# Kernel tuning notes

Hardware: AMD Instinct MI355X
Metric: run time of the kernel (lower is better)

## Reference

```python
import jax, jax.numpy as jnp
import numpy as np

N, D, E, EDGE_DIM = 8192, 64, 262144, 4


def setup_inputs() -> dict:
    key = jax.random.key(0)
    k1, k2, k3, k4, k5, k6 = jax.random.split(key, 6)
    mag = jax.random.uniform(k1, (N, D), dtype=jnp.float32)
    phase = jax.random.normal(k2, (N, D), dtype=jnp.float32)
    edge_index = jax.random.randint(k3, (2, E), 0, N, dtype=jnp.int64)
    edge_attr = jax.random.normal(k4, (E, EDGE_DIM), dtype=jnp.float32)
    # nn.Linear(edge_dim, hidden_dim): weight [hidden_dim, edge_dim], bias [hidden_dim]
    bound = 1.0 / np.sqrt(EDGE_DIM)
    W = jax.random.uniform(k5, (D, EDGE_DIM), minval=-bound, maxval=bound, dtype=jnp.float32)
    b = jax.random.uniform(k6, (D,), minval=-bound, maxval=bound, dtype=jnp.float32)
    return {"mag": mag, "phase": phase, "edge_index": edge_index,
            "edge_attr": edge_attr, "W": W, "b": b}


def reference(mag, phase, edge_index, edge_attr, W, b):
    # score_ij = sum_d mag_i[d]*mag_j[d]*cos(phase_i[d]-phase_j[d])
    # Via cos(a-b) = cos a cos b + sin a sin b -> two [N,D]@[D,N] matmuls,
    # avoiding the O(N^2 D) intermediate while computing identical math.
    c = mag * jnp.cos(phase)  # [N, D]
    s = mag * jnp.sin(phase)  # [N, D]
    scores = c @ c.T + s @ s.T  # [N, N]
    # edge bias: edge_bias[src, dst] = sum_h Linear(edge_attr)[e, h]
    edge_scores = (edge_attr @ W.T + b).sum(axis=-1)  # [E]
    bias = jnp.zeros((mag.shape[0], mag.shape[0]), dtype=scores.dtype)
    bias = bias.at[edge_index[0], edge_index[1]].set(edge_scores)
    scores = scores + bias
    attn = jax.nn.softmax(scores, axis=1)  # [N, N]
    new_mag = attn @ mag  # [N, D]
    new_phase = attn @ phase  # [N, D]
    return new_mag, new_phase
```

## Files before the change

kernel.cpp:

```cpp
#include <hip/hip_runtime.h>
#include <hip/hip_bf16.h>
#include <cstdint>

#define N_NODES 8192
#define DDIM    64
#define DX      128
#define NEDGE   262144
#define BR      128
#define BC      64
#define SPLITS  8
#define TILES   (N_NODES / BC / SPLITS)
#define RCAP    64
#define MSHIFT  66.0f
#define PSTR    76

typedef float f32x4 __attribute__((ext_vector_type(4)));
typedef short short8 __attribute__((ext_vector_type(8)));

__device__ __forceinline__ short f2bf(float f) {
    union { float f; uint32_t u; } v; v.f = f;
    uint32_t u = v.u;
    uint32_t r = (u + 0x7FFFu + ((u >> 16) & 1u)) >> 16;
    return (short)r;
}
__device__ __forceinline__ float bf2f(short s) {
    union { uint32_t u; float f; } v;
    v.u = ((uint32_t)(uint16_t)s) << 16;
    return v.f;
}

__global__ void cpa_prep_all(const float* __restrict__ mag, const float* __restrict__ phase,
                             const int* __restrict__ ei, const float* __restrict__ ea,
                             const float* __restrict__ W, const float* __restrict__ b,
                             short* __restrict__ Xbf, short* __restrict__ Ybt,
                             float* __restrict__ es, int* __restrict__ cnt,
                             int* __restrict__ keys) {
    __shared__ short tile[64][65];
    __shared__ float wsb[5];
    const int blk = blockIdx.x;
    const int tid = threadIdx.x;
    if (blk < 2048) {
        int idx = blk * 256 + tid;
        int i = idx >> 6, d = idx & 63;
        float m = mag[idx], p = phase[idx];
        Xbf[i * DX + d]      = f2bf(m * __cosf(p));
        Xbf[i * DX + 64 + d] = f2bf(m * __sinf(p));
    } else if (blk < 2304) {
        int bb = blk - 2048;
        int bi = bb >> 1;
        int bc = bb & 1;
        int i0 = bi * 64;
        const float* src = bc ? phase : mag;
        for (int itr = 0; itr < 16; ++itr) {
            int idx = tid + itr * 256;
            int ii = idx >> 6, cc = idx & 63;
            tile[ii][cc] = f2bf(src[(size_t)(i0 + ii) * 64 + cc]);
        }
        __syncthreads();
        for (int itr = 0; itr < 16; ++itr) {
            int idx = tid + itr * 256;
            int cc = idx >> 6, ii = idx & 63;
            Ybt[(size_t)(bc * 64 + cc) * N_NODES + i0 + ii] = tile[ii][cc];
        }
    } else {
        if (tid < 64) {
            float w0 = W[tid * 4 + 0], w1 = W[tid * 4 + 1];
            float w2 = W[tid * 4 + 2], w3 = W[tid * 4 + 3];
            float bb = b[tid];
            #pragma unroll
            for (int o = 32; o > 0; o >>= 1) {
                w0 += __shfl_down(w0, o);
                w1 += __shfl_down(w1, o);
                w2 += __shfl_down(w2, o);
                w3 += __shfl_down(w3, o);
                bb += __shfl_down(bb, o);
            }
            if (tid == 0) { wsb[0] = w0; wsb[1] = w1; wsb[2] = w2; wsb[3] = w3; wsb[4] = bb; }
        }
        __syncthreads();
        int e = (blk - 2304) * 256 + tid;
        float4 a = *(const float4*)(ea + (size_t)e * 4);
        es[e] = a.x * wsb[0] + a.y * wsb[1] + a.z * wsb[2] + a.w * wsb[3] + wsb[4];
        int src = ei[e];
        int dst = ei[NEDGE + e];
        int pos = atomicAdd(&cnt[src], 1);
        if (pos < RCAP) keys[src * RCAP + pos] = (dst << 18) | e;
    }
}

__global__ __launch_bounds__(256) void cpa_sortrows(const int* __restrict__ cnt,
                                                    int* __restrict__ keys) {
    int row  = blockIdx.x * 4 + (threadIdx.x >> 6);
    int lane = threadIdx.x & 63;
    int len  = min(cnt[row], RCAP);
    int base = row * RCAP;
    int v = (lane < len) ? keys[base + lane] : 0x7FFFFFFF;

    #pragma unroll
    for (int k = 2; k <= 64; k <<= 1) {
        #pragma unroll
        for (int j = k >> 1; j >= 1; j >>= 1) {
            int p = __shfl_xor(v, j);
            bool asc = (lane & k) == 0;
            bool low = (lane & j) == 0;
            v = (low == asc) ? min(v, p) : max(v, p);
        }
    }
    int nxt = __shfl_down(v, 1);
    bool dead = (lane + 1 < len) && ((v >> 18) == (nxt >> 18));
    if (lane < len) keys[base + lane] = v | (dead ? 0x80000000 : 0);
}

__global__ __launch_bounds__(512) void cpa_flash(
    const short* __restrict__ Xbf, const short* __restrict__ Ybt,
    const float* __restrict__ es, const int* __restrict__ keys,
    const int* __restrict__ cnt,
    float* __restrict__ lsplit, short* __restrict__ Opart)
{
    __shared__ short Xj[BC][136];
    __shared__ short Yt[DX][72];
    __shared__ short Pl[BR][PSTR];

    const int tid   = threadIdx.x;
    const int lane  = tid & 63;
    const int w     = tid >> 6;
    const int q     = lane >> 4;
    const int colid = lane & 15;

    const int ib = blockIdx.x;
    const int split = blockIdx.y;
    const int i0 = ib * BR;
    const int jstart = split * (N_NODES / SPLITS);

    short8 afrag[4];
    #pragma unroll
    for (int kf = 0; kf < 4; ++kf)
        afrag[kf] = *(const short8*)(Xbf + (size_t)(i0 + w * 16 + colid) * DX + kf * 32 + q * 8);

    int cur = 0, rend = 0;
    if (lane < 16) {
        int i = i0 + w * 16 + lane;
        cur = i * RCAP;
        rend = cur + min(cnt[i], RCAP);
        while (cur < rend) {
            int k = keys[cur];
            int dst = (k >> 18) & 0x1FFF;
            if (dst >= jstart) break;
            ++cur;
        }
    }

    float l_r[4] = {0.f, 0.f, 0.f, 0.f};
    f32x4 O[8];
    #pragma unroll
    for (int t = 0; t < 8; ++t) O[t] = (f32x4){0.f, 0.f, 0.f, 0.f};

    for (int tt = 0; tt < TILES; ++tt) {
        const int j0 = jstart + tt * BC;
        for (int itr = 0; itr < 2; ++itr) {
            int idx = tid + itr * 512;
            int r = idx >> 4;
            int c8 = (idx & 15) << 3;
            *(int4*)(&Xj[r][c8]) = *(const int4*)(Xbf + (size_t)(j0 + r) * DX + c8);
        }
        for (int itr = 0; itr < 2; ++itr) {
            int idx = tid + itr * 512;
            int n = idx >> 3;
            int k8 = (idx & 7) << 3;
            *(int4*)(&Yt[n][k8]) = *(const int4*)(Ybt + (size_t)n * N_NODES + j0 + k8);
        }
        __syncthreads();

        f32x4 S[4];
        #pragma unroll
        for (int st = 0; st < 4; ++st) {
            f32x4 acc = (f32x4){0.f, 0.f, 0.f, 0.f};
            #pragma unroll
            for (int kf = 0; kf < 4; ++kf) {
                short8 bfrag = *(const short8*)&Xj[st * 16 + colid][kf * 32 + q * 8];
                acc = __builtin_amdgcn_mfma_f32_16x16x32_bf16(afrag[kf], bfrag, acc, 0, 0, 0);
            }
            S[st] = acc;
        }
        float rsum[4] = {0.f, 0.f, 0.f, 0.f};
        short pb[4][4];
        #pragma unroll
        for (int st = 0; st < 4; ++st) {
            #pragma unroll
            for (int r = 0; r < 4; ++r) {
                float p = __expf(S[st][r] - MSHIFT);
                rsum[r] += p;
                pb[st][r] = f2bf(p);
            }
        }
        #pragma unroll
        for (int r = 0; r < 4; ++r) {
            float s_ = rsum[r];
            s_ += __shfl_xor(s_, 1);
            s_ += __shfl_xor(s_, 2);
            s_ += __shfl_xor(s_, 4);
            s_ += __shfl_xor(s_, 8);
            l_r[r] += s_;
        }
        #pragma unroll
        for (int st = 0; st < 4; ++st)
            #pragma unroll
            for (int r = 0; r < 4; ++r)
                Pl[w * 16 + q * 4 + r][st * 16 + colid] = pb[st][r];

        float dlocal = 0.f;
        if (lane < 16) {
            const int jend = j0 + BC;
            int c = cur;
            while (c < rend) {
                int k = keys[c];
                int dst = (k >> 18) & 0x1FFF;
                if (dst >= jend) break;
                ++c;
                if (k >= 0) {
                    int ec = dst - j0;
                    float old = bf2f(Pl[w * 16 + lane][ec]);
                    float nw = old * __expf(es[k & 0x3FFFF]);
                    Pl[w * 16 + lane][ec] = f2bf(nw);
                    dlocal += nw - old;
                }
            }
            cur = c;
        }
        #pragma unroll
        for (int r = 0; r < 4; ++r)
            l_r[r] += __shfl(dlocal, q * 4 + r);

        short8 pf0 = *(const short8*)&Pl[w * 16 + colid][q * 8];
        short8 pf1 = *(const short8*)&Pl[w * 16 + colid][32 + q * 8];
        #pragma unroll
        for (int t = 0; t < 8; ++t) {
            short8 b0 = *(const short8*)&Yt[t * 16 + colid][q * 8];
            short8 b1 = *(const short8*)&Yt[t * 16 + colid][32 + q * 8];
            O[t] = __builtin_amdgcn_mfma_f32_16x16x32_bf16(pf0, b0, O[t], 0, 0, 0);
            O[t] = __builtin_amdgcn_mfma_f32_16x16x32_bf16(pf1, b1, O[t], 0, 0, 0);
        }
        __syncthreads();
    }

    const int ibase = i0 + w * 16 + q * 4;
    #pragma unroll
    for (int r = 0; r < 4; ++r) {
        if (colid == r)
            lsplit[(size_t)split * N_NODES + ibase + r] = l_r[r];
    }
    #pragma unroll
    for (int t = 0; t < 8; ++t) {
        #pragma unroll
        for (int r = 0; r < 4; ++r) {
            size_t off = ((size_t)split * N_NODES + ibase + r) * DX + t * 16 + colid;
            Opart[off] = f2bf(O[t][r]);
        }
    }
}

__global__ void cpa_merge(const float* __restrict__ lsplit, const short* __restrict__ Opart,
                          float* __restrict__ out) {
    int gid = blockIdx.x * 256 + threadIdx.x;
    int i = gid >> 7;
    int c = gid & 127;
    float den = 0.f, num = 0.f;
    #pragma unroll
    for (int s = 0; s < SPLITS; ++s) {
        den += lsplit[(size_t)s * N_NODES + i];
        num += bf2f(Opart[((size_t)s * N_NODES + i) * DX + c]);
    }
    float val = num / den;
    if (c < 64) out[(size_t)i * 64 + c] = val;
    else        out[(size_t)N_NODES * 64 + (size_t)i * 64 + (c - 64)] = val;
}

extern "C" void kernel_launch(void* const* d_in, const int* in_sizes, int n_in,
                              void* d_out, int out_size, void* d_ws, size_t ws_size,
                              hipStream_t stream)
{
    const float* mag   = (const float*)d_in[0];
    const float* phase = (const float*)d_in[1];
    const int*   ei    = (const int*)d_in[2];
    const float* ea    = (const float*)d_in[3];
    const float* W     = (const float*)d_in[4];
    const float* b     = (const float*)d_in[5];
    float* out = (float*)d_out;

    char* ws = (char*)d_ws;
    short* Xbf    = (short*)(ws + 0);
    short* Ybt    = (short*)(ws + 2097152);
    float* es     = (float*)(ws + 4194304);
    int*   keys   = (int*)  (ws + 5242880);
    int*   cnt    = (int*)  (ws + 7340032);
    float* lsplit = (float*)(ws + 7373056);
    short* Opart  = (short*)(ws + 7635200);

    hipMemsetAsync(cnt, 0, N_NODES * sizeof(int), stream);
    cpa_prep_all<<<2048 + 256 + NEDGE / 256, 256, 0, stream>>>(mag, phase, ei, ea, W, b,
                                                               Xbf, Ybt, es, cnt, keys);
    cpa_sortrows<<<N_NODES / 4, 256, 0, stream>>>(cnt, keys);
    cpa_flash<<<dim3(N_NODES / BR, SPLITS), 512, 0, stream>>>(Xbf, Ybt, es, keys, cnt,
                                                              lsplit, Opart);
    cpa_merge<<<N_NODES * DX / 256, 256, 0, stream>>>(lsplit, Opart, out);
}
```

Baseline: 176.7 us.

## Switch flash kernel to 32x32x16 MFMA tiles with 2D wave split and MFMA row sums

Rewrites the attention tile loop to use 32x32x16 bf16 MFMA instead of 16x16x32. The 8 waves are split into a 4x2 grid of row and column groups, so each wave computes a 32x32 block of S and a 32x64 slice of the output. The softmax denominator is now accumulated by an extra MFMA against a ones vector on the bf16 P tile, replacing the shuffle reductions and the per-edge delta tracking. This adds a __syncthreads between P construction and the PV product and sets a min-blocks launch bound. Because the denominator now comes from bf16-rounded P, it may differ slightly from the previous fp32 sum.

```diff
diff --git a/kernel.cpp b/kernel.cpp
--- a/kernel.cpp
+++ b/kernel.cpp
@@ -12,9 +12,8 @@
 #define TILES   (N_NODES / BC / SPLITS)
 #define RCAP    64
 #define MSHIFT  66.0f
-#define PSTR    76
-
-typedef float f32x4 __attribute__((ext_vector_type(4)));
+
+typedef float f32x16 __attribute__((ext_vector_type(16)));
 typedef short short8 __attribute__((ext_vector_type(8)));
 
 __device__ __forceinline__ short f2bf(float f) {
@@ -111,7 +110,7 @@
     if (lane < len) keys[base + lane] = v | (dead ? 0x80000000 : 0);
 }
 
-__global__ __launch_bounds__(512) void cpa_flash(
+__global__ __launch_bounds__(512, 4) void cpa_flash(
     const short* __restrict__ Xbf, const short* __restrict__ Ybt,
     const float* __restrict__ es, const int* __restrict__ keys,
     const int* __restrict__ cnt,
@@ -119,41 +118,46 @@
 {
     __shared__ short Xj[BC][136];
     __shared__ short Yt[DX][72];
-    __shared__ short Pl[BR][PSTR];
-
-    const int tid   = threadIdx.x;
-    const int lane  = tid & 63;
-    const int w     = tid >> 6;
-    const int q     = lane >> 4;
-    const int colid = lane & 15;
+    __shared__ short Pl[BR][72];
+
+    const int tid  = threadIdx.x;
+    const int lane = tid & 63;
+    const int w    = tid >> 6;
+    const int l31  = lane & 31;
+    const int lh   = lane >> 5;
+    const int rg   = w >> 1;
+    const int cg   = w & 1;
+    const int ocg0 = (w & 1) * 2;
 
     const int ib = blockIdx.x;
     const int split = blockIdx.y;
     const int i0 = ib * BR;
     const int jstart = split * (N_NODES / SPLITS);
 
-    short8 afrag[4];
-    #pragma unroll
-    for (int kf = 0; kf < 4; ++kf)
-        afrag[kf] = *(const short8*)(Xbf + (size_t)(i0 + w * 16 + colid) * DX + kf * 32 + q * 8);
+    short8 afrag[8];
+    #pragma unroll
+    for (int kf = 0; kf < 8; ++kf)
+        afrag[kf] = *(const short8*)(Xbf + (size_t)(i0 + rg * 32 + l31) * DX + kf * 16 + lh * 8);
+
+    short8 ones;
+    #pragma unroll
+    for (int j = 0; j < 8; ++j) ones[j] = (short)0x3F80;
 
     int cur = 0, rend = 0;
-    if (lane < 16) {
-        int i = i0 + w * 16 + lane;
+    if (lane < 32) {
+        int i = i0 + rg * 32 + l31;
         cur = i * RCAP;
         rend = cur + min(cnt[i], RCAP);
         while (cur < rend) {
             int k = keys[cur];
-            int dst = (k >> 18) & 0x1FFF;
-            if (dst >= jstart) break;
+            if (((k >> 18) & 0x1FFF) >= jstart) break;
             ++cur;
         }
     }
 
-    float l_r[4] = {0.f, 0.f, 0.f, 0.f};
-    f32x4 O[8];
-    #pragma unroll
-    for (int t = 0; t < 8; ++t) O[t] = (f32x4){0.f, 0.f, 0.f, 0.f};
+    f32x16 O0, O1, lC;
+    #pragma unroll
+    for (int r = 0; r < 16; ++r) { O0[r] = 0.f; O1[r] = 0.f; lC[r] = 0.f; }
 
     for (int tt = 0; tt < TILES; ++tt) {
         const int j0 = jstart + tt * BC;
@@ -171,46 +175,22 @@
         }
         __syncthreads();
 
-        f32x4 S[4];
-        #pragma unroll
-        for (int st = 0; st < 4; ++st) {
-            f32x4 acc = (f32x4){0.f, 0.f, 0.f, 0.f};
-            #pragma unroll
-            for (int kf = 0; kf < 4; ++kf) {
-                short8 bfrag = *(const short8*)&Xj[st * 16 + colid][kf * 32 + q * 8];
-                acc = __builtin_amdgcn_mfma_f32_16x16x32_bf16(afrag[kf], bfrag, acc, 0, 0, 0);
-            }
-            S[st] = acc;
-        }
-        float rsum[4] = {0.f, 0.f, 0.f, 0.f};
-        short pb[4][4];
-        #pragma unroll
-        for (int st = 0; st < 4; ++st) {
-            #pragma unroll
-            for (int r = 0; r < 4; ++r) {
-                float p = __expf(S[st][r] - MSHIFT);
-                rsum[r] += p;
-                pb[st][r] = f2bf(p);
-            }
-        }
-        #pragma unroll
-        for (int r = 0; r < 4; ++r) {
-            float s_ = rsum[r];
-            s_ += __shfl_xor(s_, 1);
-            s_ += __shfl_xor(s_, 2);
-            s_ += __shfl_xor(s_, 4);
-            s_ += __shfl_xor(s_, 8);
-            l_r[r] += s_;
-        }
-        #pragma unroll
-        for (int st = 0; st < 4; ++st)
-            #pragma unroll
-            for (int r = 0; r < 4; ++r)
-                Pl[w * 16 + q * 4 + r][st * 16 + colid] = pb[st][r];
-
-        float dlocal = 0.f;
-        if (lane < 16) {
+        f32x16 S;
+        #pragma unroll
+        for (int r = 0; r < 16; ++r) S[r] = 0.f;
+        #pragma unroll
+        for (int kf = 0; kf < 8; ++kf) {
+            short8 bfrag = *(const short8*)&Xj[cg * 32 + l31][kf * 16 + lh * 8];
+            S = __builtin_amdgcn_mfma_f32_32x32x16_bf16(afrag[kf], bfrag, S, 0, 0, 0);
+        }
+        #pragma unroll
+        for (int r = 0; r < 16; ++r) {
+            int rowl = 4 * lh + (r & 3) + 8 * (r >> 2);
+            Pl[rg * 32 + rowl][cg * 32 + l31] = f2bf(__expf(S[r] - MSHIFT));
+        }
+        if (lane < 32) {
             const int jend = j0 + BC;
+            const int wlo = j0 + cg * 32;
             int c = cur;
             while (c < rend) {
                 int k = keys[c];
@@ -218,43 +198,42 @@
                 if (dst >= jend) break;
                 ++c;
                 if (k >= 0) {
-                    int ec = dst - j0;
-                    float old = bf2f(Pl[w * 16 + lane][ec]);
-                    float nw = old * __expf(es[k & 0x3FFFF]);
-                    Pl[w * 16 + lane][ec] = f2bf(nw);
-                    dlocal += nw - old;
+                    unsigned cl = (unsigned)(dst - wlo);
+                    if (cl < 32u) {
+                        short* p = &Pl[rg * 32 + l31][cg * 32 + (int)cl];
+                        *p = f2bf(bf2f(*p) * __expf(es[k & 0x3FFFF]));
+                    }
                 }
             }
             cur = c;
         }
-        #pragma unroll
-        for (int r = 0; r < 4; ++r)
-            l_r[r] += __shfl(dlocal, q * 4 + r);
-
-        short8 pf0 = *(const short8*)&Pl[w * 16 + colid][q * 8];
-        short8 pf1 = *(const short8*)&Pl[w * 16 + colid][32 + q * 8];
-        #pragma unroll
-        for (int t = 0; t < 8; ++t) {
-            short8 b0 = *(const short8*)&Yt[t * 16 + colid][q * 8];
-            short8 b1 = *(const short8*)&Yt[t * 16 + colid][32 + q * 8];
-            O[t] = __builtin_amdgcn_mfma_f32_16x16x32_bf16(pf0, b0, O[t], 0, 0, 0);
-            O[t] = __builtin_amdgcn_mfma_f32_16x16x32_bf16(pf1, b1, O[t], 0, 0, 0);
-        }
-        __syncthreads();
-    }
-
-    const int ibase = i0 + w * 16 + q * 4;
-    #pragma unroll
-    for (int r = 0; r < 4; ++r) {
-        if (colid == r)
-            lsplit[(size_t)split * N_NODES + ibase + r] = l_r[r];
-    }
-    #pragma unroll
-    for (int t = 0; t < 8; ++t) {
-        #pragma unroll
-        for (int r = 0; r < 4; ++r) {
-            size_t off = ((size_t)split * N_NODES + ibase + r) * DX + t * 16 + colid;
-            Opart[off] = f2bf(O[t][r]);
+        __syncthreads();
+
+        #pragma unroll
+        for (int ks = 0; ks < 4; ++ks) {
+            short8 pa  = *(const short8*)&Pl[rg * 32 + l31][ks * 16 + lh * 8];
+            short8 yb0 = *(const short8*)&Yt[ocg0 * 32 + l31][ks * 16 + lh * 8];
+            short8 yb1 = *(const short8*)&Yt[(ocg0 + 1) * 32 + l31][ks * 16 + lh * 8];
+            O0 = __builtin_amdgcn_mfma_f32_32x32x16_bf16(pa, yb0, O0, 0, 0, 0);
+            O1 = __builtin_amdgcn_mfma_f32_32x32x16_bf16(pa, yb1, O1, 0, 0, 0);
+            if (!(w & 1))
+                lC = __builtin_amdgcn_mfma_f32_32x32x16_bf16(pa, ones, lC, 0, 0, 0);
+        }
+        __syncthreads();
+    }
+
+    #pragma unroll
+    for (int r = 0; r < 16; ++r) {
+        int row = rg * 32 + 4 * lh + (r & 3) + 8 * (r >> 2);
+        size_t base = ((size_t)split * N_NODES + i0 + row) * DX;
+        Opart[base + ocg0 * 32 + l31]       = f2bf(O0[r]);
+        Opart[base + (ocg0 + 1) * 32 + l31] = f2bf(O1[r]);
+    }
+    if (!(w & 1) && l31 == 0) {
+        #pragma unroll
+        for (int r = 0; r < 16; ++r) {
+            int row = rg * 32 + 4 * lh + (r & 3) + 8 * (r >> 2);
+            lsplit[(size_t)split * N_NODES + i0 + row] = lC[r];
         }
     }
 }
```

Result: faster. 167.8 us (-5.0%).
